# Optimization experiments

Measured on AMD Instinct MI355X. Metric: run time of the kernel, lower is better.

The kernel has to match this reference:

```python
import jax, jax.numpy as jnp
import numpy as np

BS, N, K = 256, 2048, 64
EPS = 0.1
MAX_ITER = 200
SMALL = 1e-20


def setup_inputs() -> dict:
    key = jax.random.key(0)
    k1, k2 = jax.random.split(key)
    scores = jax.random.normal(k1, (BS, N), dtype=jnp.float32)
    W = jax.random.normal(k2, (1, N, 1), dtype=jnp.float32)  # learned param of the module
    return {"scores": scores, "W": W}


def sinkhorn_forward(C, mu, nu, epsilon, max_iter):
    # C: [bs, n, k+1]; mu: [1, n, 1]; nu: [1, 1, k+1]
    bs, n, k_ = C.shape
    G = jnp.exp(-C / epsilon)
    u0 = jnp.ones((bs, n, 1), C.dtype)
    v0 = jnp.ones((bs, 1, k_), C.dtype) / k_

    def body(carry, _):
        u, v = carry
        u = mu / (G * v).sum(-1, keepdims=True)
        v = nu / (G * u).sum(-2, keepdims=True)
        return (u, v), None

    (u, v), _ = jax.lax.scan(body, (u0, v0), None, length=max_iter)
    return u * G * v  # Gamma [bs, n, k+1]


def reference(scores, W):
    bs, n = scores.shape
    s = scores[:, :, None]  # [bs, n, 1]

    # -inf masking / fill, stats are detached (stop_gradient)
    mask = jnp.isneginf(s)
    s_d = jax.lax.stop_gradient(s)
    max_s = jnp.max(s_d)
    min_s = jnp.min(jnp.where(mask, jnp.inf, s_d))
    filled = min_s - (max_s - min_s)
    s = jnp.where(mask, filled, s)

    anchors = (K - jnp.arange(K + 1, dtype=jnp.float32)).reshape(1, 1, K + 1)
    C = (s - anchors) ** 2
    C = C / jax.lax.stop_gradient(C.max())  # [bs, n, k+1]

    mu = jnp.ones((1, n, 1), jnp.float32) / n
    nu = jnp.concatenate([jnp.full((K,), 1.0 / n, jnp.float32),
                          jnp.array([(n - K) / n], jnp.float32)]).reshape(1, 1, K + 1)

    # tau = <sorted(detached scores), W>
    sorted_s = jnp.sort(jax.lax.stop_gradient(s), axis=1)
    tau = (sorted_s * W).sum(-2, keepdims=True)  # [bs, 1, 1]

    topk_val, _ = jax.lax.top_k(jax.lax.stop_gradient(s)[..., 0], K)  # [bs, K]
    Gamma0 = jax.nn.sigmoid(-jnp.abs(topk_val[:, None, :] - s) / tau) + SMALL  # [bs, n, K]
    Gamma0 = Gamma0 / Gamma0.sum(-2, keepdims=True) / n
    last = jnp.clip(1.0 / n - Gamma0.sum(-1, keepdims=True), SMALL, 1.0 - SMALL)
    Gamma0 = jnp.concatenate([Gamma0, last], axis=-1)  # [bs, n, k+1]

    # epsilon=0.1 > 0.01 -> non-stabilized path (use_iter=True)
    Gamma = sinkhorn_forward(C, mu, nu, EPS, MAX_ITER)

    A = Gamma[:, :, :K] * n  # [bs, n, k]
    return A, jnp.linalg.norm((Gamma - Gamma0).ravel())
```

## Files before the change

kernel.cpp:

```cpp
#include <hip/hip_runtime.h>
#include <math.h>

#define BS 256
#define NN 2048
#define KK 64
#define KP1 65
#define NTHREADS 1024
#define NTEAMS 256
#define ROWS_PT 8
#define NPAIRS 4
#define MAX_ITER 200
#define SLABR 32
#define SLABS 68

#define DPP_ADD(x, ctrl) ((x) + __int_as_float(__builtin_amdgcn_mov_dpp(      \
                              __float_as_int(x), (ctrl), 0xF, 0xF, true)))
#define SWZ_ADD(x, pat)  ((x) + __int_as_float(__builtin_amdgcn_ds_swizzle(   \
                              __float_as_int(x), (pat))))

typedef float f2 __attribute__((ext_vector_type(2)));

__device__ __forceinline__ f2 pk_fma(f2 a, f2 b, f2 c) {
    f2 d;
    asm("v_pk_fma_f32 %0, %1, %2, %3" : "=v"(d) : "v"(a), "v"(b), "v"(c));
    return d;
}
__device__ __forceinline__ f2 pk_mul(f2 a, f2 b) {
    f2 d;
    asm("v_pk_mul_f32 %0, %1, %2" : "=v"(d) : "v"(a), "v"(b));
    return d;
}
__device__ __forceinline__ f2 pk_add(f2 a, f2 b) {
    f2 d;
    asm("v_pk_add_f32 %0, %1, %2" : "=v"(d) : "v"(a), "v"(b));
    return d;
}
__device__ __forceinline__ f2 splat2(float b) { f2 s; s.x = b; s.y = b; return s; }

__device__ __forceinline__ unsigned enc_f32(float f) {
    unsigned b = __float_as_uint(f);
    return b ^ (unsigned)(((int)b >> 31) | (int)0x80000000);
}
__device__ __forceinline__ float dec_f32(unsigned e) {
    unsigned b = (e & 0x80000000u) ? (e & 0x7FFFFFFFu) : ~e;
    return __uint_as_float(b);
}

__global__ void minmax_kernel(const float* __restrict__ s,
                              unsigned* __restrict__ maxenc,
                              unsigned* __restrict__ minenc,
                              unsigned* __restrict__ infc) {
    int tid = blockIdx.x * blockDim.x + threadIdx.x;
    int stride = gridDim.x * blockDim.x;
    float mx = -INFINITY, mn = INFINITY;
    unsigned cnt = 0;
    for (int i = tid; i < BS * NN; i += stride) {
        float v = s[i];
        if (isinf(v) && v < 0.0f) cnt++;
        else { mx = fmaxf(mx, v); mn = fminf(mn, v); }
    }
    for (int off = 32; off > 0; off >>= 1) {
        mx = fmaxf(mx, __shfl_down(mx, off));
        mn = fminf(mn, __shfl_down(mn, off));
        cnt += __shfl_down(cnt, off);
    }
    __shared__ float smx[8], smn[8];
    __shared__ unsigned scnt[8];
    int wid = threadIdx.x >> 6, lane = threadIdx.x & 63;
    if (lane == 0) { smx[wid] = mx; smn[wid] = mn; scnt[wid] = cnt; }
    __syncthreads();
    if (threadIdx.x == 0) {
        int nw = blockDim.x >> 6;
        for (int w = 1; w < nw; w++) { mx = fmaxf(mx, smx[w]); mn = fminf(mn, smn[w]); cnt += scnt[w]; }
        atomicMax(maxenc, enc_f32(mx));
        atomicMin(minenc, enc_f32(mn));
        if (cnt) atomicAdd(infc, cnt);
    }
}

__global__ void __launch_bounds__(NTHREADS)
sink_main(const float* __restrict__ scores, const float* __restrict__ W,
          float* __restrict__ out,
          const unsigned* __restrict__ maxenc, const unsigned* __restrict__ minenc,
          const unsigned* __restrict__ infc, double* __restrict__ norm_acc)
{
    const int tid  = threadIdx.x;
    const int b    = blockIdx.x;
    const int team = tid >> 2;
    const int seg  = tid & 3;
    const int wid  = tid >> 6;
    const int lane = tid & 63;

    __shared__ float ss[NN];
    __shared__ float srt[NN];
    __shared__ float4 pairs_sh[NPAIRS * NTEAMS * 4];
    __shared__ float v_sh[68] __attribute__((aligned(16)));
    __shared__ float vprev_sh[68];
    __shared__ float slab[SLABR * SLABS] __attribute__((aligned(16)));
    __shared__ double red_sh[NTHREADS];
    __shared__ float recS_sh[KK];
    __shared__ float topk_sh[KK];

    const float LOG2E   = 1.4426950408889634f;
    const float inv_n   = 1.0f / 2048.0f;
    const float nu_last = 1984.0f / 2048.0f;

    float smax = dec_f32(*maxenc);
    float smin = dec_f32(*minenc);
    unsigned icnt = *infc;
    float filled = smin - (smax - smin);
    float slo = (icnt > 0) ? filled : smin;
    float cA = slo * slo, cB = (slo - 64.0f) * (slo - 64.0f);
    float cC = smax * smax, cD = (smax - 64.0f) * (smax - 64.0f);
    float Cmax = fmaxf(fmaxf(cA, cB), fmaxf(cC, cD));
    float negc2 = -(10.0f * LOG2E) / Cmax;
    float m2 = -2.0f * negc2;

    for (int i = tid; i < NN; i += NTHREADS) {
        float v = scores[(size_t)b * NN + i];
        if (isinf(v) && v < 0.0f) v = filled;
        ss[i] = v; srt[i] = v;
    }
    __syncthreads();

    for (int size = 2; size <= NN; size <<= 1) {
        for (int stride = size >> 1; stride > 0; stride >>= 1) {
            #pragma unroll
            for (int pp = 0; pp < (NN / 2) / NTHREADS; pp++) {
                int p = tid + pp * NTHREADS;
                int lo = ((p & ~(stride - 1)) << 1) | (p & (stride - 1));
                int hi = lo + stride;
                bool up = ((lo & size) == 0);
                float x = srt[lo], y = srt[hi];
                if ((x > y) == up) { srt[lo] = y; srt[hi] = x; }
            }
            __syncthreads();
        }
    }

    for (int k = tid; k < KK; k += NTHREADS) topk_sh[k] = srt[NN - 1 - k];

    double tp = 0.0;
    for (int i = tid; i < NN; i += NTHREADS) tp += (double)srt[i] * (double)W[i];
    red_sh[tid] = tp;
    __syncthreads();
    for (int s2 = NTHREADS / 2; s2 > 0; s2 >>= 1) {
        if (tid < s2) red_sh[tid] += red_sh[tid + s2];
        __syncthreads();
    }
    float tau = (float)red_sh[0];
    float lt = LOG2E / tau;

    if (tid < KP1) {
        float a = (float)(KK - tid);
        v_sh[tid] = __builtin_amdgcn_exp2f(negc2 * a * a) * (1.0f / 65.0f);
    }

    for (int item = tid; item < NPAIRS * NTEAMS * 4; item += NTHREADS) {
        int pr = item >> 10;
        int tm = (item >> 2) & (NTEAMS - 1);
        int sg = item & 3;
        int rowA = tm + NTEAMS * (2 * pr);
        int rowB = rowA + NTEAMS;
        float wA = __builtin_amdgcn_exp2f(m2 * ss[rowA]);
        float wB = __builtin_amdgcn_exp2f(m2 * ss[rowB]);
        float a2 = wA * wA, a4 = a2 * a2, a8 = a4 * a4, a16 = a8 * a8;
        float b2 = wB * wB, b4 = b2 * b2, b8 = b4 * b4, b16 = b8 * b8;
        float wcA = wA, wcB = wB;
        if (sg < 3) { wcA *= a16; wcB *= b16; }
        if (sg < 2) { wcA *= a16; wcB *= b16; }
        if (sg < 1) { wcA *= a16; wcB *= b16; }
        pairs_sh[item] = make_float4(wcA, wA, wcB, wB);
    }
    __syncthreads();

    const bool writer = ((lane & 0x1C) == 0);
    const int  half   = lane >> 5;
    const int  srow   = wid * 2 + half;

    {
        float tk[16];
        #pragma unroll
        for (int kk = 0; kk < 16; kk++) tk[kk] = topk_sh[seg * 16 + kk];
        float part[16];
        #pragma unroll
        for (int kk = 0; kk < 16; kk++) part[kk] = 0.0f;
        #pragma unroll 1
        for (int r = 0; r < ROWS_PT; r++) {
            float si = ss[team + NTEAMS * r];
            #pragma unroll
            for (int kk = 0; kk < 16; kk++) {
                float d = fabsf(tk[kk] - si);
                float e = __builtin_amdgcn_exp2f(d * lt);
                part[kk] += 1.0f / (1.0f + e) + 1e-20f;
            }
        }
        #pragma unroll
        for (int kk = 0; kk < 16; kk++) {
            part[kk] = SWZ_ADD(part[kk], 0x101F);
            part[kk] = DPP_ADD(part[kk], 0x128);
            part[kk] = SWZ_ADD(part[kk], 0x401F);
        }
        if (writer) {
            float4* dst = (float4*)&slab[srow * SLABS + seg * 16];
            dst[0] = make_float4(part[0], part[1], part[2], part[3]);
            dst[1] = make_float4(part[4], part[5], part[6], part[7]);
            dst[2] = make_float4(part[8], part[9], part[10], part[11]);
            dst[3] = make_float4(part[12], part[13], part[14], part[15]);
        }
    }
    __syncthreads();
    if (tid < KK) {
        float sum = 0.0f;
        #pragma unroll
        for (int g = 0; g < SLABR; g++) sum += slab[g * SLABS + tid];
        recS_sh[tid] = 1.0f / sum;
    }
    __syncthreads();

    for (int t = 0; t < MAX_ITER; t++) {
        f2 vl2[8];
        float v64;
        #pragma unroll
        for (int q = 0; q < 4; q++) {
            float4 vv = ((const float4*)(v_sh + seg * 16))[q];
            vl2[2 * q + 0].x = vv.x; vl2[2 * q + 0].y = vv.y;
            vl2[2 * q + 1].x = vv.z; vl2[2 * q + 1].y = vv.w;
        }
        v64 = v_sh[64];
        f2 cpP[8];
        #pragma unroll
        for (int p = 0; p < 8; p++) { cpP[p].x = 0.0f; cpP[p].y = 0.0f; }
        float c64 = 0.0f;

        #pragma unroll 2
        for (int pr = 0; pr < NPAIRS; pr++) {
            const float4 pw = pairs_sh[pr * (NTEAMS * 4) + team * 4 + seg];
            const float wcA = pw.x, wA = pw.y, wcB = pw.z, wB = pw.w;
            const f2 wA2p = splat2(wA * wA);
            const f2 wB2p = splat2(wB * wB);
            f2 hA2 = vl2[0], hB2 = vl2[0];
            #pragma unroll
            for (int q = 1; q < 8; q++) {
                hA2 = pk_fma(hA2, wA2p, vl2[q]);
                hB2 = pk_fma(hB2, wB2p, vl2[q]);
            }
            float hA = fmaf(hA2.x, wA, hA2.y);
            float hB = fmaf(hB2.x, wB, hB2.y);
            float pA = hA * wcA, pB = hB * wcB;
            if (seg == 3) { pA += v64; pB += v64; }
            pA = DPP_ADD(pA, 0xB1);
            pB = DPP_ADD(pB, 0xB1);
            pA = DPP_ADD(pA, 0x4E);
            pB = DPP_ADD(pB, 0x4E);
            float uA = inv_n / pA;
            float uB = inv_n / pB;
            float tclA = uA * wcA, tclB = uB * wcB;
            f2 tA, tB;
            tA.x = tclA * wA; tA.y = tclA;
            tB.x = tclB * wB; tB.y = tclB;
            #pragma unroll
            for (int p = 7; p >= 0; p--) {
                cpP[p] = pk_add(cpP[p], tA);
                cpP[p] = pk_add(cpP[p], tB);
                if (p) { tA = pk_mul(tA, wA2p); tB = pk_mul(tB, wB2p); }
            }
            if (seg == 3) c64 += uA + uB;
        }

        #pragma unroll
        for (int p = 0; p < 8; p++) {
            float lo = cpP[p].x, hi = cpP[p].y;
            lo = SWZ_ADD(lo, 0x101F); lo = DPP_ADD(lo, 0x128); lo = SWZ_ADD(lo, 0x401F);
            hi = SWZ_ADD(hi, 0x101F); hi = DPP_ADD(hi, 0x128); hi = SWZ_ADD(hi, 0x401F);
            cpP[p].x = lo; cpP[p].y = hi;
        }
        c64 = SWZ_ADD(c64, 0x101F);
        c64 = DPP_ADD(c64, 0x128);
        c64 = SWZ_ADD(c64, 0x401F);
        if (writer) {
            float4* dst = (float4*)&slab[srow * SLABS + seg * 16];
            dst[0] = make_float4(cpP[0].x, cpP[0].y, cpP[1].x, cpP[1].y);
            dst[1] = make_float4(cpP[2].x, cpP[2].y, cpP[3].x, cpP[3].y);
            dst[2] = make_float4(cpP[4].x, cpP[4].y, cpP[5].x, cpP[5].y);
            dst[3] = make_float4(cpP[6].x, cpP[6].y, cpP[7].x, cpP[7].y);
            if (seg == 3) slab[srow * SLABS + 64] = c64;
        }
        __syncthreads();
        if (tid < 8 * KP1) {
            int col = tid >> 3, r8 = tid & 7;
            float cs = slab[r8 * SLABS + col]
                     + slab[(r8 + 8)  * SLABS + col]
                     + slab[(r8 + 16) * SLABS + col]
                     + slab[(r8 + 24) * SLABS + col];
            cs = DPP_ADD(cs, 0xB1);
            cs = DPP_ADD(cs, 0x4E);
            cs = SWZ_ADD(cs, 0x101F);
            if (r8 == 0) {
                float nuj = (col == KK) ? nu_last : inv_n;
                vprev_sh[col] = v_sh[col];
                v_sh[col] = nuj / cs;
            }
        }
        __syncthreads();
    }

    {
        float vp[16], vp64;
        #pragma unroll
        for (int j = 0; j < 16; j++) vp[j] = vprev_sh[seg * 16 + j];
        vp64 = vprev_sh[64];
        #pragma unroll
        for (int pr = 0; pr < NPAIRS; pr++) {
            const float4 pw = pairs_sh[pr * (NTEAMS * 4) + team * 4 + seg];
            int rowA = team + NTEAMS * (2 * pr);
            int rowB = rowA + NTEAMS;
            float hA = vp[0], hB = vp[0];
            #pragma unroll
            for (int m = 1; m < 16; m++) {
                hA = fmaf(hA, pw.y, vp[m]);
                hB = fmaf(hB, pw.w, vp[m]);
            }
            float pA = hA * pw.x, pB = hB * pw.z;
            if (seg == 3) { pA += vp64; pB += vp64; }
            pA = DPP_ADD(pA, 0xB1); pB = DPP_ADD(pB, 0xB1);
            pA = DPP_ADD(pA, 0x4E); pB = DPP_ADD(pB, 0x4E);
            if (seg == 0) {
                srt[rowA] = inv_n / pA;
                srt[rowB] = inv_n / pB;
            }
        }
    }
    __syncthreads();

    {
        float vloc[16], v64;
        #pragma unroll
        for (int j = 0; j < 16; j++) vloc[j] = v_sh[seg * 16 + j];
        v64 = v_sh[64];

        double npart = 0.0;
        #pragma unroll 1
        for (int r = 0; r < ROWS_PT; r++) {
            int row = team + NTEAMS * r;
            int pr = r >> 1, isB = r & 1;
            const float4 pw = pairs_sh[pr * (NTEAMS * 4) + team * 4 + seg];
            float wv  = isB ? pw.w : pw.y;
            float wcv = isB ? pw.z : pw.x;
            float si = ss[row];
            float u  = srt[row];
            float gm[16];
            float ug = u * wcv;
            #pragma unroll
            for (int m = 15; m >= 0; m--) { gm[m] = ug * vloc[m]; ug *= wv; }

            float g0sum = 0.0f;
            float* orow = out + ((size_t)b * NN + row) * KK + seg * 16;
            #pragma unroll
            for (int q = 0; q < 4; q++) {
                float4 o;
                #define DO_K(kk_, fld) { const int kl = 4 * q + kk_;            \
                    float dd = fabsf(topk_sh[seg * 16 + kl] - si);              \
                    float e  = __builtin_amdgcn_exp2f(dd * lt);                 \
                    float sg = 1.0f / (1.0f + e) + 1e-20f;                      \
                    float g0 = (sg * recS_sh[seg * 16 + kl]) * inv_n;           \
                    g0sum += g0;                                                \
                    float df = gm[kl] - g0; npart += (double)df * (double)df;   \
                    o.fld = gm[kl] * 2048.0f; }
                DO_K(0, x) DO_K(1, y) DO_K(2, z) DO_K(3, w)
                #undef DO_K
                ((float4*)orow)[q] = o;
            }
            float gtot = g0sum;
            gtot = DPP_ADD(gtot, 0xB1);
            gtot = DPP_ADD(gtot, 0x4E);
            if (seg == 3) {
                float last = inv_n - gtot;
                last = fminf(fmaxf(last, 1e-20f), 1.0f - 1e-20f);
                float gm64 = u * v64;
                float df = gm64 - last;
                npart += (double)df * (double)df;
            }
        }

        __syncthreads();
        red_sh[tid] = npart;
        __syncthreads();
        for (int s2 = NTHREADS / 2; s2 > 0; s2 >>= 1) {
            if (tid < s2) red_sh[tid] += red_sh[tid + s2];
            __syncthreads();
        }
        if (tid == 0) atomicAdd(norm_acc, red_sh[0]);
    }
}

__global__ void finalize_kernel(const double* __restrict__ norm_acc, float* __restrict__ out) {
    if (threadIdx.x == 0 && blockIdx.x == 0)
        out[(size_t)BS * NN * KK] = (float)sqrt(*norm_acc);
}

extern "C" void kernel_launch(void* const* d_in, const int* in_sizes, int n_in,
                              void* d_out, int out_size, void* d_ws, size_t ws_size,
                              hipStream_t stream) {
    const float* scores = (const float*)d_in[0];
    const float* W = (const float*)d_in[1];
    float* out = (float*)d_out;

    unsigned* maxenc = (unsigned*)d_ws;
    unsigned* infc   = maxenc + 1;
    double*  nacc    = (double*)((char*)d_ws + 8);
    unsigned* minenc = (unsigned*)((char*)d_ws + 16);

    hipMemsetAsync(d_ws, 0, 16, stream);
    hipMemsetAsync((char*)d_ws + 16, 0xFF, 4, stream);

    hipLaunchKernelGGL(minmax_kernel, dim3(256), dim3(256), 0, stream,
                       scores, maxenc, minenc, infc);
    hipLaunchKernelGGL(sink_main, dim3(BS), dim3(NTHREADS), 0, stream,
                       scores, W, out, maxenc, minenc, infc, nacc);
    hipLaunchKernelGGL(finalize_kernel, dim3(1), dim3(64), 0, stream, nacc, out);
}
```

Before: 903.0 us.

## Split Sinkhorn row pass into batched denominators and shared-division column pass

The fused per-pair loop is split into two phases. The first computes all four pair denominators with packed reductions and keeps only the one each lane owns, so each lane does two divisions instead of eight. The second pass broadcasts those reciprocals across the quad with DPP and builds the column partial sums. Packed-math asm now uses in-place accumulator constraints, the first pair initialises the partials directly instead of zeroing them, and the cross-lane reductions are done as packed adds. The cost is reloading the pair weights and recomputing the squared weights in the second pass, plus a few extra DPP broadcasts.

```diff
diff --git a/kernel.cpp b/kernel.cpp
--- a/kernel.cpp
+++ b/kernel.cpp
@@ -17,18 +17,21 @@
                               __float_as_int(x), (ctrl), 0xF, 0xF, true)))
 #define SWZ_ADD(x, pat)  ((x) + __int_as_float(__builtin_amdgcn_ds_swizzle(   \
                               __float_as_int(x), (pat))))
+#define DPPF(x, ctrl) __int_as_float(__builtin_amdgcn_mov_dpp(                \
+                              __float_as_int(x), (ctrl), 0xF, 0xF, true))
+#define SWZF(x, pat)  __int_as_float(__builtin_amdgcn_ds_swizzle(             \
+                              __float_as_int(x), (pat)))
 
 typedef float f2 __attribute__((ext_vector_type(2)));
 
-__device__ __forceinline__ f2 pk_fma(f2 a, f2 b, f2 c) {
-    f2 d;
-    asm("v_pk_fma_f32 %0, %1, %2, %3" : "=v"(d) : "v"(a), "v"(b), "v"(c));
-    return d;
-}
-__device__ __forceinline__ f2 pk_mul(f2 a, f2 b) {
-    f2 d;
-    asm("v_pk_mul_f32 %0, %1, %2" : "=v"(d) : "v"(a), "v"(b));
-    return d;
+__device__ __forceinline__ void pk_fma_acc(f2& h, f2 m, f2 a) {
+    asm("v_pk_fma_f32 %0, %0, %1, %2" : "+v"(h) : "v"(m), "v"(a));
+}
+__device__ __forceinline__ void pk_add_acc(f2& acc, f2 t) {
+    asm("v_pk_add_f32 %0, %0, %1" : "+v"(acc) : "v"(t));
+}
+__device__ __forceinline__ void pk_mul_acc(f2& t, f2 m) {
+    asm("v_pk_mul_f32 %0, %0, %1" : "+v"(t) : "v"(m));
 }
 __device__ __forceinline__ f2 pk_add(f2 a, f2 b) {
     f2 d;
@@ -36,6 +39,25 @@
     return d;
 }
 __device__ __forceinline__ f2 splat2(float b) { f2 s; s.x = b; s.y = b; return s; }
+
+__device__ __forceinline__ float quad_bcast(float v, int pr) {
+    int i = __float_as_int(v), r;
+    switch (pr & 3) {
+        case 0:  r = __builtin_amdgcn_mov_dpp(i, 0x00, 0xF, 0xF, true); break;
+        case 1:  r = __builtin_amdgcn_mov_dpp(i, 0x55, 0xF, 0xF, true); break;
+        case 2:  r = __builtin_amdgcn_mov_dpp(i, 0xAA, 0xF, 0xF, true); break;
+        default: r = __builtin_amdgcn_mov_dpp(i, 0xFF, 0xF, 0xF, true); break;
+    }
+    return __int_as_float(r);
+}
+
+__device__ __forceinline__ f2 half_reduce(f2 v) {
+    f2 t;
+    t.x = SWZF(v.x, 0x101F); t.y = SWZF(v.y, 0x101F); v = pk_add(v, t);
+    t.x = DPPF(v.x, 0x128);  t.y = DPPF(v.y, 0x128);  v = pk_add(v, t);
+    t.x = SWZF(v.x, 0x401F); t.y = SWZF(v.y, 0x401F); v = pk_add(v, t);
+    return v;
+}
 
 __device__ __forceinline__ unsigned enc_f32(float f) {
     unsigned b = __float_as_uint(f);
@@ -219,62 +241,72 @@
     __syncthreads();
 
     for (int t = 0; t < MAX_ITER; t++) {
-        f2 vl2[8];
-        float v64;
-        #pragma unroll
-        for (int q = 0; q < 4; q++) {
-            float4 vv = ((const float4*)(v_sh + seg * 16))[q];
-            vl2[2 * q + 0].x = vv.x; vl2[2 * q + 0].y = vv.y;
-            vl2[2 * q + 1].x = vv.z; vl2[2 * q + 1].y = vv.w;
-        }
-        v64 = v_sh[64];
-        f2 cpP[8];
-        #pragma unroll
-        for (int p = 0; p < 8; p++) { cpP[p].x = 0.0f; cpP[p].y = 0.0f; }
-        float c64 = 0.0f;
-
-        #pragma unroll 2
+        f2 vl2[8] __attribute__((aligned(16)));
+        #pragma unroll
+        for (int q = 0; q < 4; q++)
+            ((float4*)vl2)[q] = ((const float4*)(v_sh + seg * 16))[q];
+        const float v64 = v_sh[64];
+        const f2 v64p = splat2(v64);
+
+        f2 myP = splat2(1.0f);
+        #pragma unroll
         for (int pr = 0; pr < NPAIRS; pr++) {
             const float4 pw = pairs_sh[pr * (NTEAMS * 4) + team * 4 + seg];
-            const float wcA = pw.x, wA = pw.y, wcB = pw.z, wB = pw.w;
-            const f2 wA2p = splat2(wA * wA);
-            const f2 wB2p = splat2(wB * wB);
+            const f2 wA2p = splat2(pw.y * pw.y);
+            const f2 wB2p = splat2(pw.w * pw.w);
             f2 hA2 = vl2[0], hB2 = vl2[0];
             #pragma unroll
             for (int q = 1; q < 8; q++) {
-                hA2 = pk_fma(hA2, wA2p, vl2[q]);
-                hB2 = pk_fma(hB2, wB2p, vl2[q]);
-            }
-            float hA = fmaf(hA2.x, wA, hA2.y);
-            float hB = fmaf(hB2.x, wB, hB2.y);
-            float pA = hA * wcA, pB = hB * wcB;
-            if (seg == 3) { pA += v64; pB += v64; }
-            pA = DPP_ADD(pA, 0xB1);
-            pB = DPP_ADD(pB, 0xB1);
-            pA = DPP_ADD(pA, 0x4E);
-            pB = DPP_ADD(pB, 0x4E);
-            float uA = inv_n / pA;
-            float uB = inv_n / pB;
-            float tclA = uA * wcA, tclB = uB * wcB;
+                pk_fma_acc(hA2, wA2p, vl2[q]);
+                pk_fma_acc(hB2, wB2p, vl2[q]);
+            }
+            f2 pP;
+            pP.x = fmaf(hA2.x, pw.y, hA2.y) * pw.x;
+            pP.y = fmaf(hB2.x, pw.w, hB2.y) * pw.z;
+            if (seg == 3) pP = pk_add(pP, v64p);
+            f2 tq;
+            tq.x = DPPF(pP.x, 0xB1); tq.y = DPPF(pP.y, 0xB1);
+            pP = pk_add(pP, tq);
+            tq.x = DPPF(pP.x, 0x4E); tq.y = DPPF(pP.y, 0x4E);
+            pP = pk_add(pP, tq);
+            myP.x = (seg == pr) ? pP.x : myP.x;
+            myP.y = (seg == pr) ? pP.y : myP.y;
+        }
+        const float uAm = inv_n / myP.x;
+        const float uBm = inv_n / myP.y;
+
+        f2 cpP[8];
+        float c64 = 0.0f;
+        #pragma unroll
+        for (int pr = 0; pr < NPAIRS; pr++) {
+            const float uA = quad_bcast(uAm, pr);
+            const float uB = quad_bcast(uBm, pr);
+            const float4 pw = pairs_sh[pr * (NTEAMS * 4) + team * 4 + seg];
+            const f2 wA2p = splat2(pw.y * pw.y);
+            const f2 wB2p = splat2(pw.w * pw.w);
+            float tclA = uA * pw.x, tclB = uB * pw.z;
             f2 tA, tB;
-            tA.x = tclA * wA; tA.y = tclA;
-            tB.x = tclB * wB; tB.y = tclB;
-            #pragma unroll
-            for (int p = 7; p >= 0; p--) {
-                cpP[p] = pk_add(cpP[p], tA);
-                cpP[p] = pk_add(cpP[p], tB);
-                if (p) { tA = pk_mul(tA, wA2p); tB = pk_mul(tB, wB2p); }
+            tA.x = tclA * pw.y; tA.y = tclA;
+            tB.x = tclB * pw.w; tB.y = tclB;
+            if (pr == 0) {
+                #pragma unroll
+                for (int p = 7; p >= 0; p--) {
+                    cpP[p] = pk_add(tA, tB);
+                    if (p) { pk_mul_acc(tA, wA2p); pk_mul_acc(tB, wB2p); }
+                }
+            } else {
+                #pragma unroll
+                for (int p = 7; p >= 0; p--) {
+                    pk_add_acc(cpP[p], tA);
+                    pk_add_acc(cpP[p], tB);
+                    if (p) { pk_mul_acc(tA, wA2p); pk_mul_acc(tB, wB2p); }
+                }
             }
             if (seg == 3) c64 += uA + uB;
         }
 
         #pragma unroll
-        for (int p = 0; p < 8; p++) {
-            float lo = cpP[p].x, hi = cpP[p].y;
-            lo = SWZ_ADD(lo, 0x101F); lo = DPP_ADD(lo, 0x128); lo = SWZ_ADD(lo, 0x401F);
-            hi = SWZ_ADD(hi, 0x101F); hi = DPP_ADD(hi, 0x128); hi = SWZ_ADD(hi, 0x401F);
-            cpP[p].x = lo; cpP[p].y = hi;
-        }
+        for (int p = 0; p < 8; p++) cpP[p] = half_reduce(cpP[p]);
         c64 = SWZ_ADD(c64, 0x101F);
         c64 = DPP_ADD(c64, 0x128);
         c64 = SWZ_ADD(c64, 0x401F);
```

New measurement: 829.6 us. 8.1% less time.
